# Performance work log

Measured on AMD Instinct MI355X. Metric: run time of the kernel, lower is better.

The kernel has to match this reference:

```python
import jax, jax.numpy as jnp
import numpy as np

SHAPES = ((64, 64), (32, 32), (16, 16), (8, 8))
HEADS, LV, P = 8, 4, 8


def _ln(x, g, b, eps=1e-5):
    m = x.mean(-1, keepdims=True)
    v = ((x - m) ** 2).mean(-1, keepdims=True)
    return (x - m) * jax.lax.rsqrt(v + eps) * g + b


def _sample_level(v, H, W, loc):
    # v: [B, heads, H*W, hd] value for one level; loc: [B, L, heads, P, 2] in [0,1]
    # Matches F.grid_sample(mode='bilinear', padding_mode='zeros', align_corners=False)
    x = loc[..., 0] * W - 0.5
    y = loc[..., 1] * H - 0.5
    x0 = jnp.floor(x)
    y0 = jnp.floor(y)
    B, L, hds, Pn = x.shape
    acc = 0.0
    for dx, dy in ((0, 0), (1, 0), (0, 1), (1, 1)):
        xi = x0 + dx
        yi = y0 + dy
        w = (1.0 - jnp.abs(x - xi)) * (1.0 - jnp.abs(y - yi))
        valid = (xi >= 0) & (xi < W) & (yi >= 0) & (yi < H)
        idx = (jnp.clip(yi, 0, H - 1) * W + jnp.clip(xi, 0, W - 1)).astype(jnp.int32)
        idx_r = idx.transpose(0, 2, 1, 3).reshape(B, hds, L * Pn)  # [B,heads,L*P]
        g = jnp.take_along_axis(v, idx_r[..., None], axis=2)  # [B,heads,L*P,hd]
        g = g.reshape(B, hds, L, Pn, -1).transpose(0, 2, 1, 3, 4)  # [B,L,heads,P,hd]
        acc = acc + (w * valid.astype(w.dtype))[..., None] * g
    return acc


def setup_inputs() -> dict:
    key = jax.random.key(0)
    ks = iter(jax.random.split(key, 64))
    B, d, depth, dff = 2, 256, 6, 1024
    inp = {}
    for i, (H, W) in enumerate(SHAPES):
        inp[f"src{i}"] = jax.random.normal(next(ks), (B, d, H, W), jnp.float32)
        inp[f"pos{i}"] = jax.random.normal(next(ks), (B, d, H, W), jnp.float32)
    s = 0.02
    off_dim = HEADS * LV * P * 2  # 512
    aw_dim = HEADS * LV * P  # 256
    inp["level_embed"] = jax.random.normal(next(ks), (LV, d), jnp.float32)
    inp["W_off"] = jax.random.normal(next(ks), (depth, d, off_dim), jnp.float32) * s
    inp["b_off"] = jax.random.normal(next(ks), (depth, off_dim), jnp.float32) * 0.5
    inp["W_attn"] = jax.random.normal(next(ks), (depth, d, aw_dim), jnp.float32) * s
    inp["b_attn"] = jnp.zeros((depth, aw_dim), jnp.float32)
    inp["W_val"] = jax.random.normal(next(ks), (depth, d, d), jnp.float32) * s
    inp["b_val"] = jnp.zeros((depth, d), jnp.float32)
    inp["W_out"] = jax.random.normal(next(ks), (depth, d, d), jnp.float32) * s
    inp["b_out"] = jnp.zeros((depth, d), jnp.float32)
    inp["ln1_g"] = jnp.ones((depth, d), jnp.float32)
    inp["ln1_b"] = jnp.zeros((depth, d), jnp.float32)
    inp["W1"] = jax.random.normal(next(ks), (depth, d, dff), jnp.float32) * s
    inp["b1"] = jnp.zeros((depth, dff), jnp.float32)
    inp["W2"] = jax.random.normal(next(ks), (depth, dff, d), jnp.float32) * s
    inp["b2"] = jnp.zeros((depth, d), jnp.float32)
    inp["ln2_g"] = jnp.ones((depth, d), jnp.float32)
    inp["ln2_b"] = jnp.zeros((depth, d), jnp.float32)
    return inp


def reference(src0, src1, src2, src3, pos0, pos1, pos2, pos3, level_embed,
              W_off, b_off, W_attn, b_attn, W_val, b_val, W_out, b_out,
              ln1_g, ln1_b, W1, b1, W2, b2, ln2_g, ln2_b):
    srcs = [src0, src1, src2, src3]
    poss = [pos0, pos1, pos2, pos3]
    B, d = src0.shape[0], src0.shape[1]
    hd = d // HEADS
    # flatten multi-scale maps: [B, C, H, W] -> [B, H*W, C]
    src_flat = jnp.concatenate([s.reshape(B, d, -1).transpose(0, 2, 1) for s in srcs], 1)
    pos_flat = jnp.concatenate(
        [p.reshape(B, d, -1).transpose(0, 2, 1) + level_embed[i] for i, p in enumerate(poss)], 1)
    # reference points; masks are all-False so valid_ratios == 1 (same ref for every level)
    refs = []
    for (H, W) in SHAPES:
        gy, gx = jnp.meshgrid((jnp.arange(H) + 0.5) / H, (jnp.arange(W) + 0.5) / W, indexing='ij')
        refs.append(jnp.stack([gx.reshape(-1), gy.reshape(-1)], -1))
    ref = jnp.concatenate(refs, 0)  # [L, 2]
    norm = jnp.array([[W, H] for (H, W) in SHAPES], jnp.float32)  # [LV, 2] (W_, H_)
    sizes = [H * W for (H, W) in SHAPES]
    starts = np.cumsum([0] + sizes[:-1]).tolist()
    depth = W_off.shape[0]
    L = src_flat.shape[1]
    x = src_flat
    for i in range(depth):
        # pre-norm deformable self-attention; value comes from un-normed residual stream
        x2 = _ln(x, ln1_g[i], ln1_b[i])
        q = x2 + pos_flat
        off = (q @ W_off[i] + b_off[i]).reshape(B, L, HEADS, LV, P, 2)
        attn = jax.nn.softmax((q @ W_attn[i] + b_attn[i]).reshape(B, L, HEADS, LV * P), -1)
        attn = attn.reshape(B, L, HEADS, LV, P)
        val = (x @ W_val[i] + b_val[i]).reshape(B, L, HEADS, hd).transpose(0, 2, 1, 3)  # [B,heads,L,hd]
        loc = ref[None, :, None, None, None, :] + off / norm[None, None, None, :, None, :]
        out = 0.0
        for l, (H, W) in enumerate(SHAPES):
            vl = val[:, :, starts[l]:starts[l] + sizes[l]]
            sl = _sample_level(vl, H, W, loc[:, :, :, l])  # [B,L,heads,P,hd]
            out = out + (attn[:, :, :, l, :, None] * sl).sum(3)
        out = out.reshape(B, L, d) @ W_out[i] + b_out[i]
        x = x + out
        # pre-norm FFN with exact gelu (torch default)
        x2 = _ln(x, ln2_g[i], ln2_b[i])
        x = x + jax.nn.gelu(x2 @ W1[i] + b1[i], approximate=False) @ W2[i] + b2[i]
    return x
```

## Files before the change

### kernel.cpp

```cpp
#include <hip/hip_runtime.h>
#include <hip/hip_bf16.h>
#include <math.h>

#define L_TOK 5440
#define NTOK  10880
#define D     256

typedef __attribute__((ext_vector_type(8))) short short8;
typedef __attribute__((ext_vector_type(4))) float f32x4;

__device__ __forceinline__ short f2bf(float f) {
    __hip_bfloat16 h = __float2bfloat16(f);
    return __builtin_bit_cast(short, h);
}
__device__ __forceinline__ float bf2f(short s) {
    unsigned u = ((unsigned)(unsigned short)s) << 16;
    return __builtin_bit_cast(float, u);
}

#define GLL16(gp, lp) \
    __builtin_amdgcn_global_load_lds((const __attribute__((address_space(1))) void*)(gp), \
                                     (__attribute__((address_space(3))) void*)(lp), 16, 0, 0)

__global__ __launch_bounds__(256) void flat_kernel(
    const float* __restrict__ s, const float* __restrict__ p, const float* __restrict__ le,
    float* __restrict__ x, short* __restrict__ xb, float* __restrict__ pos,
    int HW, int start, int lv)
{
    __shared__ float ts[32][33], tp[32][33];
    int b = blockIdx.z, c0 = blockIdx.y * 32, pix0 = blockIdx.x * 32;
    int tx = threadIdx.x & 31, ty = threadIdx.x >> 5;
#pragma unroll
    for (int i = 0; i < 4; ++i) {
        int c = c0 + ty + i * 8;
        size_t gi = ((size_t)b * D + c) * HW + pix0 + tx;
        ts[ty + i * 8][tx] = s[gi];
        tp[ty + i * 8][tx] = p[gi];
    }
    __syncthreads();
#pragma unroll
    for (int i = 0; i < 4; ++i) {
        int pix = pix0 + ty + i * 8;
        size_t bl = (size_t)b * L_TOK + start + pix;
        int c = c0 + tx;
        float v = ts[tx][ty + i * 8];
        x[bl * D + c]   = v;
        xb[bl * D + c]  = f2bf(v);
        pos[bl * D + c] = tp[tx][ty + i * 8] + le[lv * D + c];
    }
}

__global__ __launch_bounds__(256) void wconv_kernel(
    const float* __restrict__ W, short* __restrict__ Wt, int K, int N,
    int dstride, int rowoff)
{
    __shared__ float tile[32][33];
    int d = blockIdx.z;
    int n0 = blockIdx.x * 32, k0 = blockIdx.y * 32;
    const float* Wd = W + (size_t)d * K * N;
    short* Wtd = Wt + (size_t)d * dstride + (size_t)rowoff * K;
    int tx = threadIdx.x & 31, ty = threadIdx.x >> 5;
#pragma unroll
    for (int i = 0; i < 4; ++i)
        tile[ty + i * 8][tx] = Wd[(size_t)(k0 + ty + i * 8) * N + n0 + tx];
    __syncthreads();
#pragma unroll
    for (int i = 0; i < 4; ++i)
        Wtd[(size_t)(n0 + ty + i * 8) * K + k0 + tx] = f2bf(tile[tx][ty + i * 8]);
}

__global__ __launch_bounds__(256) void bpack_kernel(
    const float* __restrict__ boff, const float* __restrict__ batt, float* __restrict__ bqa)
{
    int i = blockIdx.x * 256 + threadIdx.x;
    if (i >= 6 * 768) return;
    int d = i / 768, c = i - d * 768;
    bqa[i] = (c < 512) ? boff[d * 512 + c] : batt[d * 256 + c - 512];
}

__global__ __launch_bounds__(256) void ln_kernel(
    const float* __restrict__ x, const float* __restrict__ g, const float* __restrict__ bta,
    const float* __restrict__ pos, short* __restrict__ out)
{
    int wid = threadIdx.x >> 6, lane = threadIdx.x & 63;
    int m = blockIdx.x * 4 + wid;
    const float* xr = x + (size_t)m * D;
    float v[4];
#pragma unroll
    for (int i = 0; i < 4; ++i) v[i] = xr[lane + i * 64];
    float s = v[0] + v[1] + v[2] + v[3];
#pragma unroll
    for (int o = 32; o; o >>= 1) s += __shfl_xor(s, o);
    float mean = s * (1.0f / D);
    float sq = 0.0f;
#pragma unroll
    for (int i = 0; i < 4; ++i) { float d = v[i] - mean; sq += d * d; }
#pragma unroll
    for (int o = 32; o; o >>= 1) sq += __shfl_xor(sq, o);
    float rstd = rsqrtf(sq * (1.0f / D) + 1e-5f);
    short* orow = out + (size_t)m * D;
#pragma unroll
    for (int i = 0; i < 4; ++i) {
        int c = lane + i * 64;
        float o = (v[i] - mean) * rstd * g[c] + bta[c];
        if (pos) o += pos[(size_t)m * D + c];
        orow[c] = f2bf(o);
    }
}

template<int BN>
__device__ __forceinline__ void mm_body64(
    const short* __restrict__ A, const short* __restrict__ Wt,
    const float* __restrict__ bias, const float* __restrict__ resid,
    float* __restrict__ Cf, short* __restrict__ Cb,
    int row0, int col0, int K, int ldc, int act, int f16out)
{
    constexpr int NW  = BN / 4;
    constexpr int NF  = NW / 16;
    constexpr int BCH = BN / 32;
    __shared__ __align__(16) short As[2][64 * 64];
    __shared__ __align__(16) short Bs[2][BN * 64];
    int tid = threadIdx.x, lane = tid & 63, w = tid >> 6;
    int l15 = lane & 15, l16 = lane >> 4;

    int a_off[4][2], b_off[NF][2];
#pragma unroll
    for (int m = 0; m < 4; ++m)
#pragma unroll
        for (int kk = 0; kk < 2; ++kk) {
            int ra = m * 16 + l15;
            a_off[m][kk] = ra * 64 + (((kk * 4 + l16) ^ (ra & 7)) << 3);
        }
#pragma unroll
    for (int n = 0; n < NF; ++n)
#pragma unroll
        for (int kk = 0; kk < 2; ++kk) {
            int rb = w * NW + n * 16 + l15;
            b_off[n][kk] = rb * 64 + (((kk * 4 + l16) ^ (rb & 7)) << 3);
        }

    int sg = (lane & 7) ^ ((lane >> 3) & 7);
    const short* ag = A  + (size_t)(row0 + w * 16 + (lane >> 3)) * K + sg * 8;
    const short* bg = Wt + (size_t)(col0 + w * NW + (lane >> 3)) * K + sg * 8;

    f32x4 acc[4][NF];
#pragma unroll
    for (int m = 0; m < 4; ++m)
#pragma unroll
        for (int n = 0; n < NF; ++n) acc[m][n] = (f32x4){0.f, 0.f, 0.f, 0.f};

    auto stage = [&](int buf, int kofs) {
#pragma unroll
        for (int c = 0; c < 2; ++c)
            GLL16(ag + (size_t)c * 8 * K + kofs, &As[buf][w * 1024 + c * 512]);
#pragma unroll
        for (int c = 0; c < BCH; ++c)
            GLL16(bg + (size_t)c * 8 * K + kofs, &Bs[buf][w * NW * 64 + c * 512]);
    };
    auto comp = [&](int buf) {
#pragma unroll
        for (int kk = 0; kk < 2; ++kk) {
            short8 af[4], bfr[NF];
#pragma unroll
            for (int m = 0; m < 4; ++m) af[m] = *(short8*)&As[buf][a_off[m][kk]];
#pragma unroll
            for (int n = 0; n < NF; ++n) bfr[n] = *(short8*)&Bs[buf][b_off[n][kk]];
#pragma unroll
            for (int m = 0; m < 4; ++m)
#pragma unroll
                for (int n = 0; n < NF; ++n)
                    acc[m][n] = __builtin_amdgcn_mfma_f32_16x16x32_bf16(af[m], bfr[n], acc[m][n], 0, 0, 0);
        }
    };

    stage(0, 0);
    __syncthreads();
    int cur = 0;
    for (int k0 = 64; k0 < K; k0 += 64) {
        stage(cur ^ 1, k0);
        comp(cur);
        __syncthreads();
        cur ^= 1;
    }
    comp(cur);

#pragma unroll
    for (int m = 0; m < 4; ++m) {
#pragma unroll
        for (int j = 0; j < 4; ++j) {
            int row = row0 + m * 16 + l16 * 4 + j;
#pragma unroll
            for (int n = 0; n < NF; ++n) {
                int col = col0 + w * NW + n * 16 + l15;
                float v = acc[m][n][j] + bias[col];
                if (act) v = 0.5f * v * (1.0f + erff(v * 0.70710678118654752f));
                if (resid) v += resid[(size_t)row * ldc + col];
                if (Cf) Cf[(size_t)row * ldc + col] = v;
                if (Cb) Cb[(size_t)row * ldc + col] =
                    f16out ? __builtin_bit_cast(short, (_Float16)v) : f2bf(v);
            }
        }
    }
}

template<int BN>
__global__ __launch_bounds__(256) void mm_kernel(
    const short* __restrict__ A, const short* __restrict__ Wt,
    const float* __restrict__ bias, const float* __restrict__ resid,
    float* __restrict__ Cf, short* __restrict__ Cb, int K, int ldc, int act)
{
    mm_body64<BN>(A, Wt, bias, resid, Cf, Cb, blockIdx.y * 64, blockIdx.x * BN, K, ldc, act, 0);
}

__global__ __launch_bounds__(256) void mm2_kernel(
    const short* __restrict__ A1, const short* __restrict__ Wt1, const float* __restrict__ bias1,
    short* __restrict__ C1, int ldc1,
    const short* __restrict__ A2, const short* __restrict__ Wt2, const float* __restrict__ bias2,
    short* __restrict__ C2, int ldc2,
    int nx1, int K)
{
    const short *A, *Wt; const float* bias; short* Cb; int ldc, col0, f16o;
    if ((int)blockIdx.x < nx1) {
        A = A1; Wt = Wt1; bias = bias1; Cb = C1; ldc = ldc1; f16o = 1;
        col0 = blockIdx.x * 128;
    } else {
        A = A2; Wt = Wt2; bias = bias2; Cb = C2; ldc = ldc2; f16o = 0;
        col0 = (blockIdx.x - nx1) * 128;
    }
    mm_body64<128>(A, Wt, bias, nullptr, nullptr, Cb, blockIdx.y * 64, col0, K, ldc, 0, f16o);
}

__global__ __launch_bounds__(256) void sample_kernel(
    const short* __restrict__ big, const short* __restrict__ val, short* __restrict__ out)
{
    __shared__ float sw[8 * 132];
    __shared__ int   si[8 * 132];
    int bl = blockIdx.x;
    int b = bl / L_TOK, l = bl - b * L_TOK;
    const _Float16* row = (const _Float16*)big + (size_t)bl * 768;
    int t = threadIdx.x;
    {
        int head = t >> 5, lvp = t & 31, lv = lvp >> 3, p = lvp & 7;
        int lq, r;
        if (l < 4096)      { lq = 0; r = l;        }
        else if (l < 5120) { lq = 1; r = l - 4096; }
        else if (l < 5376) { lq = 2; r = l - 5120; }
        else               { lq = 3; r = l - 5376; }
        int sh = 6 - lq;
        float invSq = 1.0f / (float)(1 << sh);
        float refx = ((r & ((1 << sh) - 1)) + 0.5f) * invSq;
        float refy = ((r >> sh) + 0.5f) * invSq;
        int S = 64 >> lv;
        int start = (lv == 0) ? 0 : (lv == 1) ? 4096 : (lv == 2) ? 5120 : 5376;
        float Sf = (float)S;
        float logit = (float)row[512 + head * 32 + lvp];
        float mx = logit;
#pragma unroll
        for (int o = 16; o; o >>= 1) mx = fmaxf(mx, __shfl_xor(mx, o));
        float e = __expf(logit - mx);
        float ssum = e;
#pragma unroll
        for (int o = 16; o; o >>= 1) ssum += __shfl_xor(ssum, o);
        float a = e / ssum;
        float ox = (float)row[head * 64 + lv * 16 + p * 2 + 0];
        float oy = (float)row[head * 64 + lv * 16 + p * 2 + 1];
        float X = refx * Sf + ox - 0.5f;
        float Y = refy * Sf + oy - 0.5f;
        float x0 = floorf(X), y0 = floorf(Y);
        float fx = X - x0, fy = Y - y0;
        int xi0 = (int)x0, yi0 = (int)y0;
        int qt = lvp >> 3, sidx = lvp & 7;
        int base_w = head * 132 + qt * 33 + sidx * 4;
#pragma unroll
        for (int tap = 0; tap < 4; ++tap) {
            int dx = tap & 1, dy = tap >> 1;
            int xi = xi0 + dx, yi = yi0 + dy;
            float wgt = (dx ? fx : 1.0f - fx) * (dy ? fy : 1.0f - fy);
            bool valid = (xi >= 0) && (xi < S) && (yi >= 0) && (yi < S);
            int xc = xi < 0 ? 0 : (xi > S - 1 ? S - 1 : xi);
            int yc = yi < 0 ? 0 : (yi > S - 1 ? S - 1 : yi);
            sw[base_w + tap] = valid ? wgt * a : 0.0f;
            si[base_w + tap] = (start + yc * S + xc) << 8;
        }
    }
    __syncthreads();
    int h = t >> 5, sgp = (t >> 2) & 7, cg = t & 3;
    const short* vb = val + (size_t)b * L_TOK * D + h * 32 + cg * 8;
    float a0 = 0.f, a1 = 0.f, a2 = 0.f, a3 = 0.f;
    float a4 = 0.f, a5 = 0.f, a6 = 0.f, a7 = 0.f;
#pragma unroll
    for (int gp = 0; gp < 2; ++gp) {
        float w8[8]; int i8[8];
#pragma unroll
        for (int ss = 0; ss < 2; ++ss) {
            int base = h * 132 + (gp * 2 + ss) * 33 + sgp * 4;
#pragma unroll
            for (int tap = 0; tap < 4; ++tap) {
                w8[ss * 4 + tap] = sw[base + tap];
                i8[ss * 4 + tap] = si[base + tap];
            }
        }
        short8 g[8];
#pragma unroll
        for (int k = 0; k < 8; ++k) g[k] = *(const short8*)&vb[i8[k]];
#pragma unroll
        for (int k = 0; k < 8; ++k) {
            float wgt = w8[k];
            a0 += wgt * bf2f(g[k][0]); a1 += wgt * bf2f(g[k][1]);
            a2 += wgt * bf2f(g[k][2]); a3 += wgt * bf2f(g[k][3]);
            a4 += wgt * bf2f(g[k][4]); a5 += wgt * bf2f(g[k][5]);
            a6 += wgt * bf2f(g[k][6]); a7 += wgt * bf2f(g[k][7]);
        }
    }
#pragma unroll
    for (int o = 4; o <= 16; o <<= 1) {
        a0 += __shfl_xor(a0, o); a1 += __shfl_xor(a1, o);
        a2 += __shfl_xor(a2, o); a3 += __shfl_xor(a3, o);
        a4 += __shfl_xor(a4, o); a5 += __shfl_xor(a5, o);
        a6 += __shfl_xor(a6, o); a7 += __shfl_xor(a7, o);
    }
    if (sgp == 0) {
        short8 o;
        o[0] = f2bf(a0); o[1] = f2bf(a1); o[2] = f2bf(a2); o[3] = f2bf(a3);
        o[4] = f2bf(a4); o[5] = f2bf(a5); o[6] = f2bf(a6); o[7] = f2bf(a7);
        *(short8*)&out[(size_t)bl * D + h * 32 + cg * 8] = o;
    }
}

extern "C" void kernel_launch(void* const* d_in, const int* in_sizes, int n_in,
                              void* d_out, int out_size, void* d_ws, size_t ws_size,
                              hipStream_t stream)
{
    const float* s0    = (const float*)d_in[0];
    const float* p0    = (const float*)d_in[1];
    const float* s1    = (const float*)d_in[2];
    const float* p1    = (const float*)d_in[3];
    const float* s2    = (const float*)d_in[4];
    const float* p2    = (const float*)d_in[5];
    const float* s3    = (const float*)d_in[6];
    const float* p3    = (const float*)d_in[7];
    const float* lvl   = (const float*)d_in[8];
    const float* W_off = (const float*)d_in[9];
    const float* b_off = (const float*)d_in[10];
    const float* W_att = (const float*)d_in[11];
    const float* b_att = (const float*)d_in[12];
    const float* W_val = (const float*)d_in[13];
    const float* b_val = (const float*)d_in[14];
    const float* W_out = (const float*)d_in[15];
    const float* b_out = (const float*)d_in[16];
    const float* ln1g  = (const float*)d_in[17];
    const float* ln1b  = (const float*)d_in[18];
    const float* W1    = (const float*)d_in[19];
    const float* b1    = (const float*)d_in[20];
    const float* W2    = (const float*)d_in[21];
    const float* b2    = (const float*)d_in[22];
    const float* ln2g  = (const float*)d_in[23];
    const float* ln2b  = (const float*)d_in[24];

    const size_t S1 = (size_t)NTOK * D;
    float* xbuf = (float*)d_ws;
    float* pos  = xbuf + S1;
    float* bigf = pos + S1;
    float* bqa  = bigf + 3 * S1;
    short* big  = (short*)bigf;
    short* qbf   = (short*)(bqa + 6 * 768);
    short* x_bf  = qbf + S1;
    short* valbf = x_bf + S1;
    short* sampb = valbf + S1;
    short* hidbf = sampb + S1;
    short* wt_qa  = hidbf + 4 * S1;
    short* wt_val = wt_qa  + (size_t)6 * 768 * 256;
    short* wt_out = wt_val + (size_t)6 * 256 * 256;
    short* wt_1   = wt_out + (size_t)6 * 256 * 256;
    short* wt_2   = wt_1   + (size_t)6 * 1024 * 256;

    wconv_kernel<<<dim3(16, 8, 6), 256, 0, stream>>>(W_off, wt_qa, 256, 512, 768 * 256, 0);
    wconv_kernel<<<dim3(8, 8, 6),  256, 0, stream>>>(W_att, wt_qa, 256, 256, 768 * 256, 512);
    wconv_kernel<<<dim3(8, 8, 6),  256, 0, stream>>>(W_val, wt_val, 256, 256, 256 * 256, 0);
    wconv_kernel<<<dim3(8, 8, 6),  256, 0, stream>>>(W_out, wt_out, 256, 256, 256 * 256, 0);
    wconv_kernel<<<dim3(32, 8, 6), 256, 0, stream>>>(W1,    wt_1,   256, 1024, 1024 * 256, 0);
    wconv_kernel<<<dim3(8, 32, 6), 256, 0, stream>>>(W2,    wt_2,   1024, 256, 256 * 1024, 0);
    bpack_kernel<<<18, 256, 0, stream>>>(b_off, b_att, bqa);

    flat_kernel<<<dim3(128, 8, 2), 256, 0, stream>>>(s0, p0, lvl, xbuf, x_bf, pos, 4096, 0, 0);
    flat_kernel<<<dim3(32, 8, 2),  256, 0, stream>>>(s1, p1, lvl, xbuf, x_bf, pos, 1024, 4096, 1);
    flat_kernel<<<dim3(8, 8, 2),   256, 0, stream>>>(s2, p2, lvl, xbuf, x_bf, pos, 256, 5120, 2);
    flat_kernel<<<dim3(2, 8, 2),   256, 0, stream>>>(s3, p3, lvl, xbuf, x_bf, pos, 64, 5376, 3);

    for (int i = 0; i < 6; ++i) {
        ln_kernel<<<NTOK / 4, 256, 0, stream>>>(xbuf, ln1g + i * 256, ln1b + i * 256, pos, qbf);
        mm2_kernel<<<dim3(8, 170), 256, 0, stream>>>(
            qbf, wt_qa + (size_t)i * 768 * 256, bqa + i * 768, big, 768,
            x_bf, wt_val + (size_t)i * 256 * 256, b_val + i * 256, valbf, 256,
            6, 256);
        sample_kernel<<<NTOK, 256, 0, stream>>>(big, valbf, sampb);
        mm_kernel<64><<<dim3(4, 170), 256, 0, stream>>>(
            sampb, wt_out + (size_t)i * 256 * 256, b_out + i * 256, xbuf, xbuf, nullptr, 256, 256, 0);
        ln_kernel<<<NTOK / 4, 256, 0, stream>>>(xbuf, ln2g + i * 256, ln2b + i * 256, nullptr, qbf);
        mm_kernel<128><<<dim3(8, 170), 256, 0, stream>>>(
            qbf, wt_1 + (size_t)i * 1024 * 256, b1 + i * 1024, nullptr, nullptr, hidbf, 256, 1024, 1);
        float* outp = (i == 5) ? (float*)d_out : xbuf;
        short* xbp  = (i == 5) ? nullptr : x_bf;
        mm_kernel<64><<<dim3(4, 170), 256, 0, stream>>>(
            hidbf, wt_2 + (size_t)i * 256 * 1024, b2 + i * 256, xbuf, outp, xbp, 1024, 256, 0);
    }
}
```

Measured before the change: 778.3 us.

## Fuse LayerNorm into full-row output GEMMs and remap sample block order

```diff
diff --git a/kernel.cpp b/kernel.cpp
--- a/kernel.cpp
+++ b/kernel.cpp
@@ -230,12 +230,116 @@
     mm_body64<128>(A, Wt, bias, nullptr, nullptr, Cb, blockIdx.y * 64, col0, K, ldc, 0, f16o);
 }
 
+__global__ __launch_bounds__(256) void mmln_kernel(
+    const short* __restrict__ A, const short* __restrict__ Wt,
+    const float* __restrict__ bias, const float* __restrict__ resid,
+    float* __restrict__ xout, short* __restrict__ xbf,
+    const float* __restrict__ g, const float* __restrict__ bta,
+    const float* __restrict__ pos, short* __restrict__ qout, int K)
+{
+    __shared__ __align__(16) char pool[34 * 1024];
+    short* As = (short*)pool;
+    short* Bs = (short*)(pool + 2048);
+    float* xs = (float*)pool;
+
+    int tid = threadIdx.x, lane = tid & 63, w = tid >> 6;
+    int l15 = lane & 15, l16 = lane >> 4;
+    int row0 = blockIdx.x * 16;
+
+    int a_off = l15 * 32 + ((l16 ^ (l15 & 3)) << 3);
+    int b_off[4];
+#pragma unroll
+    for (int n = 0; n < 4; ++n) {
+        int rb = w * 64 + n * 16 + l15;
+        b_off[n] = rb * 32 + ((l16 ^ (rb & 3)) << 3);
+    }
+    int sg4 = (lane & 3) ^ ((lane >> 2) & 3);
+    const short* ag = A  + (size_t)(row0 + (lane >> 2)) * K + sg4 * 8;
+    const short* bg = Wt + (size_t)(w * 64 + (lane >> 2)) * K + sg4 * 8;
+
+    f32x4 acc[4];
+#pragma unroll
+    for (int n = 0; n < 4; ++n) acc[n] = (f32x4){0.f, 0.f, 0.f, 0.f};
+
+    auto stage = [&](int buf, int kofs) {
+        if (w == 0) GLL16(ag + kofs, &As[buf * 512]);
+#pragma unroll
+        for (int c = 0; c < 4; ++c)
+            GLL16(bg + (size_t)c * 16 * K + kofs, &Bs[buf * 8192 + w * 2048 + c * 512]);
+    };
+    auto comp = [&](int buf) {
+        short8 af = *(short8*)&As[buf * 512 + a_off];
+#pragma unroll
+        for (int n = 0; n < 4; ++n) {
+            short8 bf8 = *(short8*)&Bs[buf * 8192 + b_off[n]];
+            acc[n] = __builtin_amdgcn_mfma_f32_16x16x32_bf16(af, bf8, acc[n], 0, 0, 0);
+        }
+    };
+
+    stage(0, 0);
+    __syncthreads();
+    int cur = 0;
+    for (int k0 = 32; k0 < K; k0 += 32) {
+        stage(cur ^ 1, k0);
+        comp(cur);
+        __syncthreads();
+        cur ^= 1;
+    }
+    comp(cur);
+    __syncthreads();
+
+#pragma unroll
+    for (int j = 0; j < 4; ++j) {
+        int lrow = l16 * 4 + j;
+        int row = row0 + lrow;
+#pragma unroll
+        for (int n = 0; n < 4; ++n) {
+            int col = w * 64 + n * 16 + l15;
+            float v = acc[n][j] + bias[col];
+            if (resid) v += resid[(size_t)row * D + col];
+            xout[(size_t)row * D + col] = v;
+            xs[lrow * 264 + col] = v;
+        }
+    }
+    if (!qout) return;
+    __syncthreads();
+
+#pragma unroll
+    for (int i = 0; i < 4; ++i) {
+        int lrow = w * 4 + i;
+        int grow = row0 + lrow;
+        float v0 = xs[lrow * 264 + lane];
+        float v1 = xs[lrow * 264 + lane + 64];
+        float v2 = xs[lrow * 264 + lane + 128];
+        float v3 = xs[lrow * 264 + lane + 192];
+        float s = v0 + v1 + v2 + v3;
+#pragma unroll
+        for (int o = 32; o; o >>= 1) s += __shfl_xor(s, o);
+        float mean = s * (1.0f / D);
+        float d0 = v0 - mean, d1 = v1 - mean, d2 = v2 - mean, d3 = v3 - mean;
+        float sq = d0 * d0 + d1 * d1 + d2 * d2 + d3 * d3;
+#pragma unroll
+        for (int o = 32; o; o >>= 1) sq += __shfl_xor(sq, o);
+        float rstd = rsqrtf(sq * (1.0f / D) + 1e-5f);
+        float vv[4] = {v0, v1, v2, v3};
+#pragma unroll
+        for (int k = 0; k < 4; ++k) {
+            int c = lane + k * 64;
+            float o = (vv[k] - mean) * rstd * g[c] + bta[c];
+            if (pos) o += pos[(size_t)grow * D + c];
+            qout[(size_t)grow * D + c] = f2bf(o);
+            if (xbf) xbf[(size_t)grow * D + c] = f2bf(vv[k]);
+        }
+    }
+}
+
 __global__ __launch_bounds__(256) void sample_kernel(
     const short* __restrict__ big, const short* __restrict__ val, short* __restrict__ out)
 {
     __shared__ float sw[8 * 132];
     __shared__ int   si[8 * 132];
-    int bl = blockIdx.x;
+    int bid = blockIdx.x;
+    int bl = (bid & 7) * 1360 + (bid >> 3);
     int b = bl / L_TOK, l = bl - b * L_TOK;
     const _Float16* row = (const _Float16*)big + (size_t)bl * 768;
     int t = threadIdx.x;
@@ -300,16 +404,16 @@
                 i8[ss * 4 + tap] = si[base + tap];
             }
         }
-        short8 g[8];
-#pragma unroll
-        for (int k = 0; k < 8; ++k) g[k] = *(const short8*)&vb[i8[k]];
+        short8 gv[8];
+#pragma unroll
+        for (int k = 0; k < 8; ++k) gv[k] = *(const short8*)&vb[i8[k]];
 #pragma unroll
         for (int k = 0; k < 8; ++k) {
             float wgt = w8[k];
-            a0 += wgt * bf2f(g[k][0]); a1 += wgt * bf2f(g[k][1]);
-            a2 += wgt * bf2f(g[k][2]); a3 += wgt * bf2f(g[k][3]);
-            a4 += wgt * bf2f(g[k][4]); a5 += wgt * bf2f(g[k][5]);
-            a6 += wgt * bf2f(g[k][6]); a7 += wgt * bf2f(g[k][7]);
+            a0 += wgt * bf2f(gv[k][0]); a1 += wgt * bf2f(gv[k][1]);
+            a2 += wgt * bf2f(gv[k][2]); a3 += wgt * bf2f(gv[k][3]);
+            a4 += wgt * bf2f(gv[k][4]); a5 += wgt * bf2f(gv[k][5]);
+            a6 += wgt * bf2f(gv[k][6]); a7 += wgt * bf2f(gv[k][7]);
         }
     }
 #pragma unroll
@@ -387,21 +491,27 @@
     flat_kernel<<<dim3(8, 8, 2),   256, 0, stream>>>(s2, p2, lvl, xbuf, x_bf, pos, 256, 5120, 2);
     flat_kernel<<<dim3(2, 8, 2),   256, 0, stream>>>(s3, p3, lvl, xbuf, x_bf, pos, 64, 5376, 3);
 
+    ln_kernel<<<NTOK / 4, 256, 0, stream>>>(xbuf, ln1g, ln1b, pos, qbf);
+
     for (int i = 0; i < 6; ++i) {
-        ln_kernel<<<NTOK / 4, 256, 0, stream>>>(xbuf, ln1g + i * 256, ln1b + i * 256, pos, qbf);
         mm2_kernel<<<dim3(8, 170), 256, 0, stream>>>(
             qbf, wt_qa + (size_t)i * 768 * 256, bqa + i * 768, big, 768,
             x_bf, wt_val + (size_t)i * 256 * 256, b_val + i * 256, valbf, 256,
             6, 256);
         sample_kernel<<<NTOK, 256, 0, stream>>>(big, valbf, sampb);
-        mm_kernel<64><<<dim3(4, 170), 256, 0, stream>>>(
-            sampb, wt_out + (size_t)i * 256 * 256, b_out + i * 256, xbuf, xbuf, nullptr, 256, 256, 0);
-        ln_kernel<<<NTOK / 4, 256, 0, stream>>>(xbuf, ln2g + i * 256, ln2b + i * 256, nullptr, qbf);
+        mmln_kernel<<<NTOK / 16, 256, 0, stream>>>(
+            sampb, wt_out + (size_t)i * 256 * 256, b_out + i * 256, xbuf,
+            xbuf, nullptr, ln2g + i * 256, ln2b + i * 256, nullptr, qbf, 256);
         mm_kernel<128><<<dim3(8, 170), 256, 0, stream>>>(
             qbf, wt_1 + (size_t)i * 1024 * 256, b1 + i * 1024, nullptr, nullptr, hidbf, 256, 1024, 1);
-        float* outp = (i == 5) ? (float*)d_out : xbuf;
-        short* xbp  = (i == 5) ? nullptr : x_bf;
-        mm_kernel<64><<<dim3(4, 170), 256, 0, stream>>>(
-            hidbf, wt_2 + (size_t)i * 256 * 1024, b2 + i * 256, xbuf, outp, xbp, 1024, 256, 0);
-    }
-}
+        if (i < 5) {
+            mmln_kernel<<<NTOK / 16, 256, 0, stream>>>(
+                hidbf, wt_2 + (size_t)i * 256 * 1024, b2 + i * 256, xbuf,
+                xbuf, x_bf, ln1g + (i + 1) * 256, ln1b + (i + 1) * 256, pos, qbf, 1024);
+        } else {
+            mmln_kernel<<<NTOK / 16, 256, 0, stream>>>(
+                hidbf, wt_2 + (size_t)i * 256 * 1024, b2 + i * 256, xbuf,
+                (float*)d_out, nullptr, nullptr, nullptr, nullptr, nullptr, 1024);
+        }
+    }
+}
```

After: 806.4 us. 1.04x slower.
